# Optimization experiments

Hardware: AMD Instinct MI355X
Metric: run time of the kernel (lower is better)

The kernel has to match this reference:

```python
import jax, jax.numpy as jnp
import numpy as np

DIM = 1024
HEADS = 16
HEAD_DIM = DIM // HEADS
SCALE = HEAD_DIM ** -0.5


def setup_inputs() -> dict:
    key = jax.random.key(0)
    k1, k2, k3, k4 = jax.random.split(key, 4)
    x = jax.random.normal(k1, (8, 1024, DIM), dtype=jnp.float32)
    # nn.Linear weight is [out, in]; init ~ small values
    W_qkv = jax.random.normal(k2, (3 * DIM, DIM), dtype=jnp.float32) * 0.02
    W_proj = jax.random.normal(k3, (DIM, DIM), dtype=jnp.float32) * 0.02
    b_proj = jax.random.normal(k4, (DIM,), dtype=jnp.float32) * 0.02
    return {"x": x, "W_qkv": W_qkv, "W_proj": W_proj, "b_proj": b_proj}


def reference(x, W_qkv, W_proj, b_proj):
    b, n, _ = x.shape
    h, d = HEADS, HEAD_DIM
    qkv = x @ W_qkv.T  # [b, n, 3*dim]
    # rearrange 'b n (qkv h d) -> qkv b h n d'
    qkv = qkv.reshape(b, n, 3, h, d).transpose(2, 0, 3, 1, 4)
    q, k, v = qkv[0], qkv[1], qkv[2]  # each [b, h, n, d]
    dots = jnp.einsum('bhid,bhjd->bhij', q, k) * SCALE
    attn = jax.nn.softmax(dots, axis=-1)
    out = jnp.einsum('bhij,bhjd->bhid', attn, v)
    out = out.transpose(0, 2, 1, 3).reshape(b, n, h * d)  # b n (h d)
    return out @ W_proj.T + b_proj
```

## Files before the change

kernel.cpp:

```cpp
#include <hip/hip_runtime.h>
#include <math.h>

#define DIM   1024
#define HEADS 16
#define HDIM  64
#define SEQ   1024
#define BATCH 8
#define QSCALE 0.1803368801111204f
#define LDH   72
#define ABM   128

typedef __attribute__((ext_vector_type(8))) short          short8_t;
typedef __attribute__((ext_vector_type(8))) unsigned short ushort8_t;
typedef __attribute__((ext_vector_type(4))) unsigned short ushort4_t;
typedef __attribute__((ext_vector_type(4))) float          floatx4;

__device__ __forceinline__ unsigned short f2bf(float f) {
    unsigned u = __float_as_uint(f);
    u += 0x7fffu + ((u >> 16) & 1u);
    return (unsigned short)(u >> 16);
}
__device__ __forceinline__ unsigned rnd_bf(float f) {
    unsigned u = __float_as_uint(f);
    return u + 0x7fffu + ((u >> 16) & 1u);
}
__device__ __forceinline__ float fast_exp2(float x) {
#if __has_builtin(__builtin_amdgcn_exp2f)
    return __builtin_amdgcn_exp2f(x);
#else
    return exp2f(x);
#endif
}
__device__ __forceinline__ void glds16(const unsigned short* g, unsigned short* l) {
    __builtin_amdgcn_global_load_lds(
        (const __attribute__((address_space(1))) void*)g,
        (__attribute__((address_space(3))) void*)l, 16, 0, 0);
}

__global__ __launch_bounds__(256) void cvt_bf16_all(const float* __restrict__ x,
                                                    const float* __restrict__ wqkv,
                                                    const float* __restrict__ wproj,
                                                    unsigned short* __restrict__ x_o,
                                                    unsigned short* __restrict__ wqkv_o,
                                                    unsigned short* __restrict__ wproj_o) {
    const int N8_X = BATCH * SEQ * DIM / 8;
    const int N8_WQ = 3 * DIM * DIM / 8;
    const int N8_WP = DIM * DIM / 8;
    int i = blockIdx.x * 256 + threadIdx.x;
    const float* in;
    unsigned short* out;
    if (i < N8_X)               { in = x;     out = x_o; }
    else if (i < N8_X + N8_WQ)  { i -= N8_X;  in = wqkv; out = wqkv_o; }
    else                        { i -= N8_X + N8_WQ;
                                  if (i >= N8_WP) return;
                                  in = wproj; out = wproj_o; }
    const float4* p = (const float4*)in + (size_t)i * 2;
    float4 a = p[0], b = p[1];
    ushort8_t u;
    u[0] = f2bf(a.x); u[1] = f2bf(a.y); u[2] = f2bf(a.z); u[3] = f2bf(a.w);
    u[4] = f2bf(b.x); u[5] = f2bf(b.y); u[6] = f2bf(b.z); u[7] = f2bf(b.w);
    ((ushort8_t*)out)[i] = u;
}

template<int MODE>
__global__ __launch_bounds__(256) void gemm_nt_mfma(const unsigned short* __restrict__ A,
                                                    const unsigned short* __restrict__ B,
                                                    const float* __restrict__ bias,
                                                    void* __restrict__ Cout,
                                                    unsigned short* __restrict__ vt,
                                                    int M, int N, int K) {
    __shared__ __align__(16) unsigned short As[128 * 64];
    __shared__ __align__(16) unsigned short Bs[128 * 64];

    const int tid  = threadIdx.x;
    const int lane = tid & 63;
    const int wave = tid >> 6;
    const int wm = (wave >> 1) * 64;
    const int wn = (wave & 1) * 64;
    const size_t brow = (size_t)blockIdx.x * 128;
    const size_t bcol = (size_t)blockIdx.y * 128;

    const int srow   = lane >> 3;
    const int schunk = (lane & 7) ^ srow;
    const unsigned short* gA = A + (brow + wave * 8 + srow) * (size_t)K + schunk * 8;
    const unsigned short* gB = B + (bcol + wave * 8 + srow) * (size_t)K + schunk * 8;
    unsigned short* lA = &As[wave * 512 + lane * 8];
    unsigned short* lB = &Bs[wave * 512 + lane * 8];

    floatx4 acc[4][4];
    #pragma unroll
    for (int i = 0; i < 4; i++)
        #pragma unroll
        for (int j = 0; j < 4; j++) acc[i][j] = (floatx4){0.f, 0.f, 0.f, 0.f};

    const int g  = lane >> 4;
    const int rr = lane & 15;
    const int xr = rr & 7;

    for (int k0 = 0; k0 < K; k0 += 64) {
        __syncthreads();
        #pragma unroll
        for (int r = 0; r < 4; r++) {
            glds16(gA + (size_t)r * 32 * K + k0, lA + r * 2048);
            glds16(gB + (size_t)r * 32 * K + k0, lB + r * 2048);
        }
        __syncthreads();

        #pragma unroll
        for (int kc = 0; kc < 2; kc++) {
            const int ch = ((kc * 4 + g) ^ xr) * 8;
            short8_t af[4], bfr[4];
            #pragma unroll
            for (int mi = 0; mi < 4; mi++)
                af[mi] = *(const short8_t*)&As[(wm + mi * 16 + rr) * 64 + ch];
            #pragma unroll
            for (int ni = 0; ni < 4; ni++)
                bfr[ni] = *(const short8_t*)&Bs[(wn + ni * 16 + rr) * 64 + ch];
            #pragma unroll
            for (int mi = 0; mi < 4; mi++)
                #pragma unroll
                for (int ni = 0; ni < 4; ni++)
                    acc[mi][ni] = __builtin_amdgcn_mfma_f32_16x16x32_bf16(
                        af[mi], bfr[ni], acc[mi][ni], 0, 0, 0);
        }
    }

    const int crow = (lane >> 4) * 4;
    const int ccol = lane & 15;

    if (MODE == 0) {
        #pragma unroll
        for (int mi = 0; mi < 4; mi++)
            #pragma unroll
            for (int ni = 0; ni < 4; ni++) {
                const size_t col = bcol + wn + ni * 16 + ccol;
                const float bv = bias[col];
                #pragma unroll
                for (int r = 0; r < 4; r++) {
                    const size_t row = brow + wm + mi * 16 + crow + r;
                    ((float*)Cout)[row * N + col] = acc[mi][ni][r] + bv;
                }
            }
    } else {
        if (bcol < 2048) {
            const float sc = (bcol < 1024) ? QSCALE : 1.0f;
            unsigned short* qk = (unsigned short*)Cout;
            #pragma unroll
            for (int mi = 0; mi < 4; mi++)
                #pragma unroll
                for (int ni = 0; ni < 4; ni++) {
                    const size_t col = bcol + wn + ni * 16 + ccol;
                    #pragma unroll
                    for (int r = 0; r < 4; r++) {
                        const size_t row = brow + wm + mi * 16 + crow + r;
                        qk[row * 2048 + col] = f2bf(acc[mi][ni][r] * sc);
                    }
                }
        } else {
            #pragma unroll
            for (int mi = 0; mi < 4; mi++)
                #pragma unroll
                for (int ni = 0; ni < 4; ni++) {
                    const int dall = (int)(bcol + wn + ni * 16 + ccol) - 2048;
                    const int h = dall >> 6, d = dall & 63;
                    const size_t row0 = brow + wm + mi * 16 + crow;
                    const size_t bb = row0 >> 10;
                    const int n0 = (int)(row0 & 1023);
                    ushort4_t o;
                    #pragma unroll
                    for (int r = 0; r < 4; r++) o[r] = f2bf(acc[mi][ni][r]);
                    *(ushort4_t*)&vt[(((size_t)bb * HEADS + h) * HDIM + d) * SEQ + n0] = o;
                }
        }
    }
}

__global__ __launch_bounds__(256) void attn_mfma(const unsigned short* __restrict__ qk,
                                                 const unsigned short* __restrict__ vt,
                                                 unsigned short* __restrict__ aout) {
    const int bh = blockIdx.x;
    const int qt = blockIdx.y;
    const int h  = bh & 15;
    const int b  = bh >> 4;
    const int tid  = threadIdx.x;
    const int lane = tid & 63;
    const int wave = tid >> 6;
    const int g = lane >> 4;
    const int c = lane & 15;

    __shared__ __align__(16) unsigned short Qs[ABM * LDH];
    __shared__ __align__(16) unsigned short Ks[2][64 * 64];
    __shared__ __align__(16) unsigned short Vs[2][64 * 64];
    __shared__ float scr[4][2][16];

    const int sr = tid >> 2;
    const int sq = tid & 3;
    const int sx = sr & 7;
    const unsigned short* ksrc0 =
        qk + ((size_t)(b * SEQ + sr)) * 2048 + DIM + h * HDIM + sq * 16;
    const unsigned short* vsrc0 =
        vt + (((size_t)(b * HEADS + h)) * HDIM + sr) * SEQ + sq * 16;
    const int kvo0 = sr * 64 + (((sq * 2)     ^ sx) * 8);
    const int kvo1 = sr * 64 + (((sq * 2 + 1) ^ sx) * 8);

    ushort8_t ck0 = *(const ushort8_t*)ksrc0;
    ushort8_t ck1 = *(const ushort8_t*)(ksrc0 + 8);
    ushort8_t cv0 = *(const ushort8_t*)vsrc0;
    ushort8_t cv1 = *(const ushort8_t*)(vsrc0 + 8);

    {
        const int r  = tid >> 1;
        const int c0 = (tid & 1) * 32;
        const unsigned short* src =
            qk + ((size_t)(b * SEQ + qt * ABM + r)) * 2048 + h * HDIM + c0;
        unsigned short* dst = &Qs[r * LDH + c0];
        *(ushort8_t*)(dst)      = *(const ushort8_t*)(src);
        *(ushort8_t*)(dst + 8)  = *(const ushort8_t*)(src + 8);
        *(ushort8_t*)(dst + 16) = *(const ushort8_t*)(src + 16);
        *(ushort8_t*)(dst + 24) = *(const ushort8_t*)(src + 24);
    }
    __syncthreads();

    short8_t bq[2][2];
    #pragma unroll
    for (int f = 0; f < 2; f++)
        #pragma unroll
        for (int kc = 0; kc < 2; kc++)
            bq[f][kc] = *(const short8_t*)&Qs[(f * 64 + wave * 16 + c) * LDH + g * 8 + kc * 32];

    floatx4 O[2][4];
    #pragma unroll
    for (int f = 0; f < 2; f++)
        #pragma unroll
        for (int i = 0; i < 4; i++) O[f][i] = (floatx4){0.f, 0.f, 0.f, 0.f};
    float lsum[2] = {0.f, 0.f};

    const int fro0 = ((0 * 4 + g) ^ (c & 7)) * 8;
    const int fro1 = ((1 * 4 + g) ^ (c & 7)) * 8;

    for (int kt = 0; kt < SEQ / 64; kt++) {
        const int cur = kt & 1;
        *(ushort8_t*)&Ks[cur][kvo0] = ck0;
        *(ushort8_t*)&Ks[cur][kvo1] = ck1;
        *(ushort8_t*)&Vs[cur][kvo0] = cv0;
        *(ushort8_t*)&Vs[cur][kvo1] = cv1;
        if (kt + 1 < SEQ / 64) {
            const unsigned short* ks = ksrc0 + (size_t)(kt + 1) * 64 * 2048;
            const unsigned short* vs = vsrc0 + (kt + 1) * 64;
            ck0 = *(const ushort8_t*)ks;
            ck1 = *(const ushort8_t*)(ks + 8);
            cv0 = *(const ushort8_t*)vs;
            cv1 = *(const ushort8_t*)(vs + 8);
        }
        __syncthreads();

        short8_t ak[4][2];
        #pragma unroll
        for (int nt = 0; nt < 4; nt++) {
            ak[nt][0] = *(const short8_t*)&Ks[cur][(nt * 16 + c) * 64 + fro0];
            ak[nt][1] = *(const short8_t*)&Ks[cur][(nt * 16 + c) * 64 + fro1];
        }

        floatx4 S[2][4];
        #pragma unroll
        for (int f = 0; f < 2; f++)
            #pragma unroll
            for (int nt = 0; nt < 4; nt++) S[f][nt] = (floatx4){0.f, 0.f, 0.f, 0.f};
        #pragma unroll
        for (int f = 0; f < 2; f++)
            #pragma unroll
            for (int nt = 0; nt < 4; nt++)
                #pragma unroll
                for (int kc = 0; kc < 2; kc++)
                    S[f][nt] = __builtin_amdgcn_mfma_f32_16x16x32_bf16(
                        ak[nt][kc], bq[f][kc], S[f][nt], 0, 0, 0);

        #pragma unroll
        for (int f = 0; f < 2; f++)
            #pragma unroll
            for (int nt = 0; nt < 4; nt++) {
                const float p0 = fast_exp2(S[f][nt][0]);
                const float p1 = fast_exp2(S[f][nt][1]);
                const float p2 = fast_exp2(S[f][nt][2]);
                const float p3 = fast_exp2(S[f][nt][3]);
                lsum[f] += (p0 + p1) + (p2 + p3);
                const unsigned r01 = __builtin_amdgcn_perm(rnd_bf(p1), rnd_bf(p0), 0x07060302);
                const unsigned r23 = __builtin_amdgcn_perm(rnd_bf(p3), rnd_bf(p2), 0x07060302);
                *(uint2*)&Qs[(f * 64 + wave * 16 + c) * LDH + nt * 16 + g * 4] =
                    make_uint2(r01, r23);
            }

        short8_t bv[4][2];
        #pragma unroll
        for (int dnt = 0; dnt < 4; dnt++) {
            bv[dnt][0] = *(const short8_t*)&Vs[cur][(dnt * 16 + c) * 64 + fro0];
            bv[dnt][1] = *(const short8_t*)&Vs[cur][(dnt * 16 + c) * 64 + fro1];
        }

        #pragma unroll
        for (int f = 0; f < 2; f++) {
            short8_t ap[2];
            #pragma unroll
            for (int kc = 0; kc < 2; kc++)
                ap[kc] = *(const short8_t*)&Qs[(f * 64 + wave * 16 + c) * LDH + g * 8 + kc * 32];
            #pragma unroll
            for (int dnt = 0; dnt < 4; dnt++)
                #pragma unroll
                for (int kc = 0; kc < 2; kc++)
                    O[f][dnt] = __builtin_amdgcn_mfma_f32_16x16x32_bf16(
                        ap[kc], bv[dnt][kc], O[f][dnt], 0, 0, 0);
        }
    }

    #pragma unroll
    for (int f = 0; f < 2; f++) {
        float s = lsum[f];
        s += __shfl_xor(s, 16);
        s += __shfl_xor(s, 32);
        if (g == 0) scr[wave][f][c] = 1.0f / s;
    }
    __builtin_amdgcn_s_waitcnt(0);

    #pragma unroll
    for (int f = 0; f < 2; f++) {
        const float4 inv4 = *(const float4*)&scr[wave][f][g * 4];
        #pragma unroll
        for (int r = 0; r < 4; r++) {
            const float invl = ((const float*)&inv4)[r];
            const size_t row = (size_t)b * SEQ + qt * ABM + f * 64 + wave * 16 + g * 4 + r;
            #pragma unroll
            for (int dnt = 0; dnt < 4; dnt++)
                aout[row * DIM + h * HDIM + dnt * 16 + c] = f2bf(O[f][dnt][r] * invl);
        }
    }
}

extern "C" void kernel_launch(void* const* d_in, const int* in_sizes, int n_in,
                              void* d_out, int out_size, void* d_ws, size_t ws_size,
                              hipStream_t stream) {
    const float* x      = (const float*)d_in[0];
    const float* W_qkv  = (const float*)d_in[1];
    const float* W_proj = (const float*)d_in[2];
    const float* b_proj = (const float*)d_in[3];
    float* out = (float*)d_out;

    const int M = BATCH * SEQ;

    unsigned short* ws       = (unsigned short*)d_ws;
    unsigned short* x_bf     = ws;
    unsigned short* wqkv_bf  = x_bf + (size_t)M * DIM;
    unsigned short* wproj_bf = wqkv_bf + (size_t)3 * DIM * DIM;
    unsigned short* qk_bf    = wproj_bf + (size_t)DIM * DIM;
    unsigned short* vt_bf    = qk_bf + (size_t)M * 2048;
    unsigned short* aout_bf  = vt_bf + (size_t)BATCH * HEADS * HDIM * SEQ;

    {
        const int n8 = (M * DIM + 3 * DIM * DIM + DIM * DIM) / 8;
        cvt_bf16_all<<<(n8 + 255) / 256, 256, 0, stream>>>(
            x, W_qkv, W_proj, x_bf, wqkv_bf, wproj_bf);
    }

    gemm_nt_mfma<2><<<dim3(M / 128, 3 * DIM / 128), 256, 0, stream>>>(
        x_bf, wqkv_bf, nullptr, qk_bf, vt_bf, M, 3 * DIM, DIM);

    attn_mfma<<<dim3(BATCH * HEADS, SEQ / ABM), 256, 0, stream>>>(qk_bf, vt_bf, aout_bf);

    gemm_nt_mfma<0><<<dim3(M / 128, DIM / 128), 256, 0, stream>>>(
        aout_bf, wproj_bf, b_proj, out, nullptr, M, DIM, DIM);
}
```

Before: 232.2 us.

## Double-buffer GEMM LDS tiles and move attention barrier ahead of prefetch

After: 233.9 us. No clear change (+0.8%).

```diff
diff --git a/kernel.cpp b/kernel.cpp
--- a/kernel.cpp
+++ b/kernel.cpp
@@ -69,8 +69,8 @@
                                                     void* __restrict__ Cout,
                                                     unsigned short* __restrict__ vt,
                                                     int M, int N, int K) {
-    __shared__ __align__(16) unsigned short As[128 * 64];
-    __shared__ __align__(16) unsigned short Bs[128 * 64];
+    __shared__ __align__(16) unsigned short As[2][128 * 32];
+    __shared__ __align__(16) unsigned short Bs[2][128 * 32];
 
     const int tid  = threadIdx.x;
     const int lane = tid & 63;
@@ -80,12 +80,13 @@
     const size_t brow = (size_t)blockIdx.x * 128;
     const size_t bcol = (size_t)blockIdx.y * 128;
 
-    const int srow   = lane >> 3;
-    const int schunk = (lane & 7) ^ srow;
-    const unsigned short* gA = A + (brow + wave * 8 + srow) * (size_t)K + schunk * 8;
-    const unsigned short* gB = B + (bcol + wave * 8 + srow) * (size_t)K + schunk * 8;
-    unsigned short* lA = &As[wave * 512 + lane * 8];
-    unsigned short* lB = &Bs[wave * 512 + lane * 8];
+    const int srow = lane >> 2;
+    const int sch  = (lane & 3) ^ (srow & 3);
+    const unsigned short* gA0 = A + (brow + wave * 16 + srow) * (size_t)K + sch * 8;
+    const unsigned short* gA1 = gA0 + (size_t)64 * K;
+    const unsigned short* gB0 = B + (bcol + wave * 16 + srow) * (size_t)K + sch * 8;
+    const unsigned short* gB1 = gB0 + (size_t)64 * K;
+    const int lofs = wave * 512 + lane * 8;
 
     floatx4 acc[4][4];
     #pragma unroll
@@ -95,34 +96,39 @@
 
     const int g  = lane >> 4;
     const int rr = lane & 15;
-    const int xr = rr & 7;
-
-    for (int k0 = 0; k0 < K; k0 += 64) {
+    const int ch = (g ^ (rr & 3)) * 8;
+
+    glds16(gA0, &As[0][lofs]);
+    glds16(gA1, &As[0][lofs + 2048]);
+    glds16(gB0, &Bs[0][lofs]);
+    glds16(gB1, &Bs[0][lofs + 2048]);
+
+    const int NIT = K >> 5;
+    for (int it = 0; it < NIT; it++) {
+        const int cur = it & 1;
         __syncthreads();
-        #pragma unroll
-        for (int r = 0; r < 4; r++) {
-            glds16(gA + (size_t)r * 32 * K + k0, lA + r * 2048);
-            glds16(gB + (size_t)r * 32 * K + k0, lB + r * 2048);
-        }
-        __syncthreads();
-
-        #pragma unroll
-        for (int kc = 0; kc < 2; kc++) {
-            const int ch = ((kc * 4 + g) ^ xr) * 8;
-            short8_t af[4], bfr[4];
-            #pragma unroll
-            for (int mi = 0; mi < 4; mi++)
-                af[mi] = *(const short8_t*)&As[(wm + mi * 16 + rr) * 64 + ch];
+        if (it + 1 < NIT) {
+            const int k0 = (it + 1) << 5;
+            glds16(gA0 + k0, &As[1 - cur][lofs]);
+            glds16(gA1 + k0, &As[1 - cur][lofs + 2048]);
+            glds16(gB0 + k0, &Bs[1 - cur][lofs]);
+            glds16(gB1 + k0, &Bs[1 - cur][lofs + 2048]);
+        }
+
+        short8_t af[4], bfr[4];
+        #pragma unroll
+        for (int mi = 0; mi < 4; mi++)
+            af[mi] = *(const short8_t*)&As[cur][(wm + mi * 16 + rr) * 32 + ch];
+        #pragma unroll
+        for (int ni = 0; ni < 4; ni++)
+            bfr[ni] = *(const short8_t*)&Bs[cur][(wn + ni * 16 + rr) * 32 + ch];
+
+        #pragma unroll
+        for (int mi = 0; mi < 4; mi++)
             #pragma unroll
             for (int ni = 0; ni < 4; ni++)
-                bfr[ni] = *(const short8_t*)&Bs[(wn + ni * 16 + rr) * 64 + ch];
-            #pragma unroll
-            for (int mi = 0; mi < 4; mi++)
-                #pragma unroll
-                for (int ni = 0; ni < 4; ni++)
-                    acc[mi][ni] = __builtin_amdgcn_mfma_f32_16x16x32_bf16(
-                        af[mi], bfr[ni], acc[mi][ni], 0, 0, 0);
-        }
+                acc[mi][ni] = __builtin_amdgcn_mfma_f32_16x16x32_bf16(
+                    af[mi], bfr[ni], acc[mi][ni], 0, 0, 0);
     }
 
     const int crow = (lane >> 4) * 4;
@@ -244,6 +250,7 @@
         *(ushort8_t*)&Ks[cur][kvo1] = ck1;
         *(ushort8_t*)&Vs[cur][kvo0] = cv0;
         *(ushort8_t*)&Vs[cur][kvo1] = cv1;
+        __syncthreads();
         if (kt + 1 < SEQ / 64) {
             const unsigned short* ks = ksrc0 + (size_t)(kt + 1) * 64 * 2048;
             const unsigned short* vs = vsrc0 + (kt + 1) * 64;
@@ -252,7 +259,6 @@
             cv0 = *(const ushort8_t*)vs;
             cv1 = *(const ushort8_t*)(vs + 8);
         }
-        __syncthreads();
 
         short8_t ak[4][2];
         #pragma unroll
```

## Switch GEMM tiles to 32x32x16 MFMA and move attention barrier before prefetch

Applied to the files above, without the earlier changes.

New measurement: 234.2 us. No clear change (+0.9%).

```diff
diff --git a/kernel.cpp b/kernel.cpp
--- a/kernel.cpp
+++ b/kernel.cpp
@@ -10,10 +10,11 @@
 #define LDH   72
 #define ABM   128
 
-typedef __attribute__((ext_vector_type(8))) short          short8_t;
-typedef __attribute__((ext_vector_type(8))) unsigned short ushort8_t;
-typedef __attribute__((ext_vector_type(4))) unsigned short ushort4_t;
-typedef __attribute__((ext_vector_type(4))) float          floatx4;
+typedef __attribute__((ext_vector_type(8)))  short          short8_t;
+typedef __attribute__((ext_vector_type(8)))  unsigned short ushort8_t;
+typedef __attribute__((ext_vector_type(4)))  unsigned short ushort4_t;
+typedef __attribute__((ext_vector_type(4)))  float          floatx4;
+typedef __attribute__((ext_vector_type(16))) float          floatx16;
 
 __device__ __forceinline__ unsigned short f2bf(float f) {
     unsigned u = __float_as_uint(f);
@@ -87,15 +88,17 @@
     unsigned short* lA = &As[wave * 512 + lane * 8];
     unsigned short* lB = &Bs[wave * 512 + lane * 8];
 
-    floatx4 acc[4][4];
-    #pragma unroll
-    for (int i = 0; i < 4; i++)
-        #pragma unroll
-        for (int j = 0; j < 4; j++) acc[i][j] = (floatx4){0.f, 0.f, 0.f, 0.f};
-
-    const int g  = lane >> 4;
-    const int rr = lane & 15;
-    const int xr = rr & 7;
+    floatx16 acc[2][2];
+    #pragma unroll
+    for (int i = 0; i < 2; i++)
+        #pragma unroll
+        for (int j = 0; j < 2; j++)
+            #pragma unroll
+            for (int r = 0; r < 16; r++) acc[i][j][r] = 0.f;
+
+    const int c32  = lane & 31;
+    const int half = lane >> 5;
+    const int xr   = c32 & 7;
 
     for (int k0 = 0; k0 < K; k0 += 64) {
         __syncthreads();
@@ -107,37 +110,29 @@
         __syncthreads();
 
         #pragma unroll
-        for (int kc = 0; kc < 2; kc++) {
-            const int ch = ((kc * 4 + g) ^ xr) * 8;
-            short8_t af[4], bfr[4];
-            #pragma unroll
-            for (int mi = 0; mi < 4; mi++)
-                af[mi] = *(const short8_t*)&As[(wm + mi * 16 + rr) * 64 + ch];
-            #pragma unroll
-            for (int ni = 0; ni < 4; ni++)
-                bfr[ni] = *(const short8_t*)&Bs[(wn + ni * 16 + rr) * 64 + ch];
-            #pragma unroll
-            for (int mi = 0; mi < 4; mi++)
-                #pragma unroll
-                for (int ni = 0; ni < 4; ni++)
-                    acc[mi][ni] = __builtin_amdgcn_mfma_f32_16x16x32_bf16(
-                        af[mi], bfr[ni], acc[mi][ni], 0, 0, 0);
-        }
-    }
-
-    const int crow = (lane >> 4) * 4;
-    const int ccol = lane & 15;
+        for (int s = 0; s < 4; s++) {
+            const int ch = ((s * 2 + half) ^ xr) * 8;
+            short8_t a0 = *(const short8_t*)&As[(wm + c32) * 64 + ch];
+            short8_t a1 = *(const short8_t*)&As[(wm + 32 + c32) * 64 + ch];
+            short8_t b0 = *(const short8_t*)&Bs[(wn + c32) * 64 + ch];
+            short8_t b1 = *(const short8_t*)&Bs[(wn + 32 + c32) * 64 + ch];
+            acc[0][0] = __builtin_amdgcn_mfma_f32_32x32x16_bf16(a0, b0, acc[0][0], 0, 0, 0);
+            acc[0][1] = __builtin_amdgcn_mfma_f32_32x32x16_bf16(a0, b1, acc[0][1], 0, 0, 0);
+            acc[1][0] = __builtin_amdgcn_mfma_f32_32x32x16_bf16(a1, b0, acc[1][0], 0, 0, 0);
+            acc[1][1] = __builtin_amdgcn_mfma_f32_32x32x16_bf16(a1, b1, acc[1][1], 0, 0, 0);
+        }
+    }
 
     if (MODE == 0) {
         #pragma unroll
-        for (int mi = 0; mi < 4; mi++)
-            #pragma unroll
-            for (int ni = 0; ni < 4; ni++) {
-                const size_t col = bcol + wn + ni * 16 + ccol;
+        for (int mi = 0; mi < 2; mi++)
+            #pragma unroll
+            for (int ni = 0; ni < 2; ni++) {
+                const size_t col = bcol + wn + ni * 32 + c32;
                 const float bv = bias[col];
                 #pragma unroll
-                for (int r = 0; r < 4; r++) {
-                    const size_t row = brow + wm + mi * 16 + crow + r;
+                for (int r = 0; r < 16; r++) {
+                    const size_t row = brow + wm + mi * 32 + (r & 3) + 8 * (r >> 2) + 4 * half;
                     ((float*)Cout)[row * N + col] = acc[mi][ni][r] + bv;
                 }
             }
@@ -146,30 +141,33 @@
             const float sc = (bcol < 1024) ? QSCALE : 1.0f;
             unsigned short* qk = (unsigned short*)Cout;
             #pragma unroll
-            for (int mi = 0; mi < 4; mi++)
-                #pragma unroll
-                for (int ni = 0; ni < 4; ni++) {
-                    const size_t col = bcol + wn + ni * 16 + ccol;
+            for (int mi = 0; mi < 2; mi++)
+                #pragma unroll
+                for (int ni = 0; ni < 2; ni++) {
+                    const size_t col = bcol + wn + ni * 32 + c32;
                     #pragma unroll
-                    for (int r = 0; r < 4; r++) {
-                        const size_t row = brow + wm + mi * 16 + crow + r;
+                    for (int r = 0; r < 16; r++) {
+                        const size_t row = brow + wm + mi * 32 + (r & 3) + 8 * (r >> 2) + 4 * half;
                         qk[row * 2048 + col] = f2bf(acc[mi][ni][r] * sc);
                     }
                 }
         } else {
             #pragma unroll
-            for (int mi = 0; mi < 4; mi++)
-                #pragma unroll
-                for (int ni = 0; ni < 4; ni++) {
-                    const int dall = (int)(bcol + wn + ni * 16 + ccol) - 2048;
+            for (int mi = 0; mi < 2; mi++)
+                #pragma unroll
+                for (int ni = 0; ni < 2; ni++) {
+                    const int dall = (int)(bcol + wn + ni * 32 + c32) - 2048;
                     const int h = dall >> 6, d = dall & 63;
-                    const size_t row0 = brow + wm + mi * 16 + crow;
-                    const size_t bb = row0 >> 10;
-                    const int n0 = (int)(row0 & 1023);
-                    ushort4_t o;
                     #pragma unroll
-                    for (int r = 0; r < 4; r++) o[r] = f2bf(acc[mi][ni][r]);
-                    *(ushort4_t*)&vt[(((size_t)bb * HEADS + h) * HDIM + d) * SEQ + n0] = o;
+                    for (int rg = 0; rg < 4; rg++) {
+                        const size_t row0 = brow + wm + mi * 32 + rg * 8 + 4 * half;
+                        const size_t bb = row0 >> 10;
+                        const int n0 = (int)(row0 & 1023);
+                        ushort4_t o;
+                        #pragma unroll
+                        for (int q = 0; q < 4; q++) o[q] = f2bf(acc[mi][ni][rg * 4 + q]);
+                        *(ushort4_t*)&vt[(((size_t)bb * HEADS + h) * HDIM + d) * SEQ + n0] = o;
+                    }
                 }
         }
     }
@@ -244,6 +242,7 @@
         *(ushort8_t*)&Ks[cur][kvo1] = ck1;
         *(ushort8_t*)&Vs[cur][kvo0] = cv0;
         *(ushort8_t*)&Vs[cur][kvo1] = cv1;
+        __syncthreads();
         if (kt + 1 < SEQ / 64) {
             const unsigned short* ks = ksrc0 + (size_t)(kt + 1) * 64 * 2048;
             const unsigned short* vs = vsrc0 + (kt + 1) * 64;
@@ -252,7 +251,6 @@
             cv0 = *(const ushort8_t*)vs;
             cv1 = *(const ushort8_t*)(vs + 8);
         }
-        __syncthreads();
 
         short8_t ak[4][2];
         #pragma unroll
```
